# Optimization experiments

Measured on AMD Instinct MI355X. Metric: run time of the kernel, lower is better.

Reference implementation:

```python
import jax, jax.numpy as jnp
import numpy as np

N_PRO, N_WAT, E = 60000, 40000, 1000000
N = N_PRO + N_WAT
IN_DIM, HID, HEADS = 21, 32, 4
EDGE_K, EDGE_DIM = 32, 32
RADIUS_MAX = 5.0
FF_HID, OUT_DIM = 128, 2
HC = HID * HEADS


def setup_inputs() -> dict:
    key = jax.random.key(0)
    ks = jax.random.split(key, 32)

    def glorot(k, shape):
        fan = shape[0] + shape[-1]
        return jax.random.normal(k, shape, jnp.float32) * jnp.sqrt(2.0 / fan)

    inp = {
        'protein_pos': jax.random.normal(ks[0], (N_PRO, 3), jnp.float32),
        'water_pos': jax.random.normal(ks[1], (N_WAT, 3), jnp.float32),
        'protein_features': jax.random.uniform(ks[2], (N_PRO, IN_DIM), jnp.float32),
        'edge_index': jax.random.randint(ks[3], (2, E), 0, N, jnp.int64),
        'gamma': jnp.array([10.0], jnp.float32),
        # feature_emb
        'Wf': glorot(ks[4], (IN_DIM, HID)), 'bf': jnp.zeros((HID,), jnp.float32),
        # edge_emb
        'We': glorot(ks[5], (EDGE_K, EDGE_DIM)), 'be': jnp.zeros((EDGE_DIM,), jnp.float32),
        # conv1 (in: HID)
        'W1': glorot(ks[6], (HID, HC)),
        'att_src1': glorot(ks[7], (HEADS, HID)), 'att_dst1': glorot(ks[8], (HEADS, HID)),
        'Wedge1': glorot(ks[9], (EDGE_DIM, HC)), 'att_edge1': glorot(ks[10], (HEADS, HID)),
        'b1': jnp.zeros((HC,), jnp.float32),
        # conv2 (in: HC)
        'W2': glorot(ks[11], (HC, HC)),
        'att_src2': glorot(ks[12], (HEADS, HID)), 'att_dst2': glorot(ks[13], (HEADS, HID)),
        'Wedge2': glorot(ks[14], (EDGE_DIM, HC)), 'att_edge2': glorot(ks[15], (HEADS, HID)),
        'b2': jnp.zeros((HC,), jnp.float32),
        # mlp
        'Wm1': glorot(ks[16], (HC, FF_HID)), 'bm1': jnp.zeros((FF_HID,), jnp.float32),
        'Wm2': glorot(ks[17], (FF_HID, OUT_DIM)), 'bm2': jnp.zeros((OUT_DIM,), jnp.float32),
    }
    return inp


def gat_conv(h, edge_attr, src, dst, W, att_s, att_d, Wedge, att_e, b):
    # h: [N, Din] -> x: [N, H, C]; edge features only modulate attention logits.
    x = (h @ W).reshape(N, HEADS, HID)
    e = (edge_attr @ Wedge).reshape(-1, HEADS, HID)
    a_s = jnp.einsum('nhc,hc->nh', x, att_s)   # [N,H]
    a_d = jnp.einsum('nhc,hc->nh', x, att_d)   # [N,H]
    a_e = jnp.einsum('ehc,hc->eh', e, att_e)   # [E,H]
    alpha = jax.nn.leaky_relu(a_s[src] + a_d[dst] + a_e, 0.2)  # [E,H]
    # segment softmax over incoming edges of each dst node
    m = jax.ops.segment_max(alpha, dst, num_segments=N)
    m = jnp.where(jnp.isfinite(m), m, 0.0)
    ex = jnp.exp(alpha - m[dst])
    den = jax.ops.segment_sum(ex, dst, num_segments=N)
    coef = ex / (den[dst] + 1e-16)             # [E,H]
    msg = x[src] * coef[:, :, None]            # [E,H,C]
    out = jax.ops.segment_sum(msg, dst, num_segments=N)  # [N,H,C]
    return out.reshape(N, HC) + b


def reference(protein_pos, water_pos, protein_features, edge_index, gamma,
              Wf, bf, We, be,
              W1, att_src1, att_dst1, Wedge1, att_edge1, b1,
              W2, att_src2, att_dst2, Wedge2, att_edge2, b2,
              Wm1, bm1, Wm2, bm2):
    pos = jnp.concatenate([protein_pos, water_pos], axis=0)  # [N,3]
    src, dst = edge_index[0], edge_index[1]
    edge_vec = pos[dst] - pos[src]
    edge_dis = jnp.linalg.norm(edge_vec, axis=-1)            # [E]
    # RBF expansion of distances
    centers = jnp.linspace(0.0, RADIUS_MAX, EDGE_K)
    edge_h = jnp.exp(-gamma[0] * (edge_dis[:, None] - centers[None, :]) ** 2)  # [E,K]
    edge_attr = edge_h @ We + be                             # [E,EDGE_DIM]

    # water nodes get one-hot 'water' feature in last slot
    water_feat = jnp.zeros((N_WAT, IN_DIM), protein_features.dtype).at[:, -1].set(1.0)
    feats = jnp.concatenate([protein_features, water_feat], axis=0)
    h = feats @ Wf + bf                                      # [N,HID]

    h = jax.nn.elu(gat_conv(h, edge_attr, src, dst, W1, att_src1, att_dst1, Wedge1, att_edge1, b1))
    h = jax.nn.elu(gat_conv(h, edge_attr, src, dst, W2, att_src2, att_dst2, Wedge2, att_edge2, b2))

    h = jax.nn.relu(h @ Wm1 + bm1) @ Wm2 + bm2               # [N,OUT_DIM]
    return h[N_PRO:]                                         # water nodes only
```

## Files before the change

kernel.cpp:

```cpp
#include <hip/hip_runtime.h>
#include <hip/hip_fp16.h>
#include <stdint.h>

#define N_PRO 60000
#define N_WAT 40000
#define NN    100000
#define NNP   100032
#define NE    1000000
#define IN_DIM 21
#define HID    32
#define HEADS  4
#define HC     128
#define EDGE_K 32
#define LUTN   2048
#define NH0B  ((NNP * 32) / 256)
#define NBUCK 196
#define EPT   4
#define SCATB ((NE / EPT + 255) / 256)
#define FCAP  6144
#define SLOTS (NBUCK * FCAP)
#define GSTRIDE 16

typedef _Float16 half8 __attribute__((ext_vector_type(8)));
typedef float    f32x4 __attribute__((ext_vector_type(4)));

__global__ __launch_bounds__(256) void k_pre(
    const float* We, const float* be,
    const float* Wedge1, const float* atte1,
    const float* Wedge2, const float* atte2,
    const float* Wf, const float* bfv,
    const float* W1, const float* atts1, const float* attd1,
    const float* gamma,
    float* smallw, float* lut, __half* w1h, int* gcur)
{
    __shared__ float V[2][128];
    __shared__ float aebs[4];
    int t = threadIdx.x;
    if (blockIdx.x == 16) {
        {
            int l = t >> 7, dh = t & 127, d = dh >> 2, h = dh & 3;
            const float* Wg = l ? Wedge2 : Wedge1;
            const float* ae = l ? atte2 : atte1;
            float s = 0.f;
            for (int c = 0; c < HID; c++)
                s += Wg[d * HC + h * HID + c] * ae[h * HID + c];
            V[l][dh] = s;
        }
        __syncthreads();
        {
            int l = t >> 7, kh = t & 127, k = kh >> 2, h = kh & 3;
            float s = 0.f;
            for (int d = 0; d < 32; d++)
                s += We[k * 32 + d] * V[l][d * 4 + h];
            smallw[(l ? 132 : 0) + kh] = s;
        }
        if (t < 8) {
            int l = t >> 2, h = t & 3;
            float s = 0.f;
            for (int d = 0; d < 32; d++)
                s += be[d] * V[l][d * 4 + h];
            smallw[(l ? 260 : 128) + h] = s;
        }
        if (t >= 32 && t < 64) {
            int c = t - 32;
            smallw[264 + c] = Wf[20 * 32 + c] + bfv[c];
        }
        {
            int side = t >> 7;
            int h = (t >> 5) & 3, c = t & 31;
            const float* av = side ? attd1 : atts1;
            float s = 0.f;
            for (int j = 0; j < 32; j++)
                s += W1[c * 128 + h * 32 + j] * av[h * 32 + j];
            smallw[(side ? 424 : 296) + (t & 127)] = s;
        }
        for (int i = t; i < 128 * 8; i += 256) {
            int c = i & 127, k4 = (i >> 7) * 4;
            float w0 = W1[(k4 + 0) * 128 + c];
            float w1v = W1[(k4 + 1) * 128 + c];
            float w2 = W1[(k4 + 2) * 128 + c];
            float w3 = W1[(k4 + 3) * 128 + c];
            __half2 p0 = __floats2half2_rn(w0, w1v);
            __half2 p1 = __floats2half2_rn(w2, w3);
            uint2 pk;
            pk.x = *(unsigned*)&p0;
            pk.y = *(unsigned*)&p1;
            *(uint2*)&w1h[c * 40 + k4] = pk;
        }
        for (int i = t; i < NBUCK * GSTRIDE; i += 256) gcur[i] = 0;
        return;
    }
    int e = blockIdx.x * 256 + t;
    int layer = e >> 11, bin = e & (LUTN - 1);
    const float* Wg = layer ? Wedge2 : Wedge1;
    const float* ae = layer ? atte2 : atte1;
    if (t < 128) {
        int d = t >> 2, h = t & 3;
        float s = 0.f;
        for (int c = 0; c < 32; c++)
            s += Wg[d * HC + h * HID + c] * ae[h * HID + c];
        V[0][t] = s;
    }
    __syncthreads();
    if (t < 128) {
        int k = t >> 2, h = t & 3;
        float s = 0.f;
        for (int d = 0; d < 32; d++)
            s += We[k * 32 + d] * V[0][d * 4 + h];
        V[1][t] = s;
    }
    if (t >= 128 && t < 132) {
        int h = t - 128;
        float s = 0.f;
        for (int d = 0; d < 32; d++)
            s += be[d] * V[0][d * 4 + h];
        aebs[h] = s;
    }
    __syncthreads();
    const float* U = V[1];
    float dd = bin * (1.0f / 256.0f);
    float g = gamma[0];
    float a0 = aebs[0], a1 = aebs[1], a2 = aebs[2], a3 = aebs[3];
    const float step = 5.0f / 31.0f;
    #pragma unroll
    for (int k = 0; k < EDGE_K; k++) {
        float tt = dd - (float)k * step;
        float r = __expf(-g * tt * tt);
        a0 += r * U[k * 4 + 0];
        a1 += r * U[k * 4 + 1];
        a2 += r * U[k * 4 + 2];
        a3 += r * U[k * 4 + 3];
    }
    *(float4*)&lut[(size_t)e * 4] = make_float4(a0, a1, a2, a3);
}

__global__ __launch_bounds__(256) void k_hs(
    const float* __restrict__ pf, const float* __restrict__ Wf,
    const float* __restrict__ bfv, const float* __restrict__ smallw,
    const int* __restrict__ ei, const float* __restrict__ ppos,
    const float* __restrict__ wpos, int* __restrict__ gcur,
    uint2* __restrict__ ebuf2,
    __half* __restrict__ h0, float* __restrict__ asd)
{
    int t = threadIdx.x;
    if (blockIdx.x < SCATB) {
        __shared__ int lh[256];
        __shared__ int lbase[256];
        lh[t] = 0;
        __syncthreads();
        int e0 = (blockIdx.x * 256 + t) * EPT;
        int bkt[EPT], rnk[EPT];
        unsigned rec0[EPT], rec1[EPT];
        #pragma unroll
        for (int j = 0; j < EPT; j++) bkt[j] = -1;
        if (e0 < NE) {
            int4 sa = *(const int4*)&ei[e0];
            int4 da = *(const int4*)&ei[NE + e0];
            int ss[4] = {sa.x, sa.y, sa.z, sa.w};
            int ds[4] = {da.x, da.y, da.z, da.w};
            #pragma unroll
            for (int j = 0; j < EPT; j++) {
                int s = ss[j], d = ds[j];
                if ((unsigned)d < (unsigned)NN) {
                    const float* ps = (s < N_PRO) ? &ppos[s * 3] : &wpos[(s - N_PRO) * 3];
                    const float* pd = (d < N_PRO) ? &ppos[d * 3] : &wpos[(d - N_PRO) * 3];
                    float dx = pd[0] - ps[0];
                    float dy = pd[1] - ps[1];
                    float dz = pd[2] - ps[2];
                    float dist = sqrtf(dx * dx + dy * dy + dz * dz);
                    unsigned code = (unsigned)fminf(dist * 4096.0f, 32767.0f);
                    bkt[j] = d >> 9;
                    rec0[j] = ((unsigned)d << 15) | code;
                    rec1[j] = (unsigned)s;
                    rnk[j] = atomicAdd(&lh[bkt[j]], 1);
                }
            }
        }
        __syncthreads();
        if (t < NBUCK)
            lbase[t] = lh[t] ? atomicAdd(&gcur[t * GSTRIDE], lh[t]) : 0;
        __syncthreads();
        #pragma unroll
        for (int j = 0; j < EPT; j++)
            if (bkt[j] >= 0) {
                int p = lbase[bkt[j]] + rnk[j];
                if (p < FCAP)
                    ebuf2[(size_t)bkt[j] * FCAP + p] = make_uint2(rec0[j], rec1[j]);
            }
        return;
    }
    __shared__ float Wfs[IN_DIM * 32];
    __shared__ float bfs[32];
    __shared__ float h0w[32];
    __shared__ float vas[128], vad[128];
    for (int i = t; i < IN_DIM * 32; i += 256) Wfs[i] = Wf[i];
    if (t < 32) { bfs[t] = bfv[t]; h0w[t] = smallw[264 + t]; }
    if (t < 128) vas[t] = smallw[296 + t];
    else         vad[t - 128] = smallw[424 + (t - 128)];
    __syncthreads();
    int id = (blockIdx.x - SCATB) * 256 + t;
    int n = id >> 5, c = id & 31;
    if (n >= NNP) return;
    float v;
    if (n < N_PRO) {
        float s = bfs[c];
        for (int k = 0; k < IN_DIM; k++)
            s += pf[n * IN_DIM + k] * Wfs[k * 32 + c];
        v = s;
    } else {
        v = h0w[c];
    }
    h0[(size_t)n * 32 + c] = __float2half(v);
    float ps[4], pd[4];
    #pragma unroll
    for (int h = 0; h < 4; h++) {
        ps[h] = v * vas[h * 32 + c];
        pd[h] = v * vad[h * 32 + c];
    }
    #pragma unroll
    for (int m = 1; m < 32; m <<= 1) {
        #pragma unroll
        for (int h = 0; h < 4; h++) {
            ps[h] += __shfl_xor(ps[h], m, 64);
            pd[h] += __shfl_xor(pd[h], m, 64);
        }
    }
    if ((t & 31) == 0) {
        *(float4*)&asd[(size_t)n * 8]     = make_float4(ps[0], ps[1], ps[2], ps[3]);
        *(float4*)&asd[(size_t)n * 8 + 4] = make_float4(pd[0], pd[1], pd[2], pd[3]);
    }
}

__global__ __launch_bounds__(1024) void k_fine(
    const int* __restrict__ gcur, const uint2* __restrict__ ebuf2,
    const float* __restrict__ lutg, const float* __restrict__ asd,
    int* __restrict__ offA, int* __restrict__ offE,
    unsigned* __restrict__ e4, float* __restrict__ wb)
{
    __shared__ uint2 eL[FCAP];
    __shared__ int lcnt[512], lexc[512];
    __shared__ int wsum[8];
    int b = blockIdx.x, t = threadIdx.x;
    int beg = b * FCAP;
    int nb = gcur[b * GSTRIDE];
    if (nb > FCAP) nb = FCAP;
    for (int i = t; i < nb; i += 1024) eL[i] = ebuf2[beg + i];
    if (t < 512) lcnt[t] = 0;
    __syncthreads();
    for (int i = t; i < nb; i += 1024)
        atomicAdd(&lcnt[(eL[i].x >> 15) & 511], 1);
    __syncthreads();
    int c = 0;
    if (t < 512) {
        c = lcnt[t];
        int lane = t & 63;
        int v = c;
        #pragma unroll
        for (int d = 1; d < 64; d <<= 1) {
            int x = __shfl_up(v, d, 64);
            if (lane >= d) v += x;
        }
        if (lane == 63) wsum[t >> 6] = v;
        lexc[t] = v - c;
    }
    __syncthreads();
    if (t < 8) {
        int orig = wsum[t];
        int v = orig;
        #pragma unroll
        for (int d = 1; d < 8; d <<= 1) {
            int x = __shfl_up(v, d, 64);
            if (t >= d) v += x;
        }
        wsum[t] = v - orig;
    }
    __syncthreads();
    if (t < 512) {
        lexc[t] += wsum[t >> 6];
        int node = b * 512 + t;
        if (node < NN) {
            offA[node] = beg + lexc[t];
            offE[node] = beg + lexc[t] + c;
        }
        lcnt[t] = 0;
    }
    __syncthreads();
    for (int i = t; i < nb; i += 1024) {
        uint2 u = eL[i];
        int ln = (int)((u.x >> 15) & 511u);
        int r = atomicAdd(&lcnt[ln], 1);
        int p = beg + lexc[ln] + r;
        unsigned code = u.x & 32767u;
        unsigned s = u.y;
        e4[p] = (s << 15) | code;
        int n = (b << 9) + ln;
        float f = fminf((float)code * 0.0625f, (float)(LUTN - 2));
        int i0 = (int)f;
        float fr = f - (float)i0;
        float4 A = *(const float4*)&lutg[(size_t)i0 * 4];
        float4 B = *(const float4*)&lutg[(size_t)(i0 + 1) * 4];
        float4 as4 = *(const float4*)&asd[(size_t)s * 8];
        float4 ad4 = *(const float4*)&asd[(size_t)n * 8 + 4];
        float v0 = as4.x + ad4.x + A.x + (B.x - A.x) * fr;
        float v1 = as4.y + ad4.y + A.y + (B.y - A.y) * fr;
        float v2 = as4.z + ad4.z + A.z + (B.z - A.z) * fr;
        float v3 = as4.w + ad4.w + A.w + (B.w - A.w) * fr;
        v0 = fmaxf(v0, 0.2f * v0);
        v1 = fmaxf(v1, 0.2f * v1);
        v2 = fmaxf(v2, 0.2f * v2);
        v3 = fmaxf(v3, 0.2f * v3);
        *(float4*)&wb[(size_t)p * 4] = make_float4(
            __expf(v0), __expf(v1), __expf(v2), __expf(v3));
    }
}

__global__ __launch_bounds__(256) void k_xm(
    const __half* __restrict__ h, const float* __restrict__ Wg,
    const float* __restrict__ atts, const float* __restrict__ attd,
    __half* __restrict__ x16, float* __restrict__ asd)
{
    __shared__ __half Wt[128 * 136];
    __shared__ float attS[128], attD[128];
    int t = threadIdx.x;
    for (int i = t; i < 128 * 32; i += 256) {
        int c = i & 127, d = (i >> 7) * 4;
        float w0 = Wg[(d + 0) * 128 + c];
        float w1 = Wg[(d + 1) * 128 + c];
        float w2 = Wg[(d + 2) * 128 + c];
        float w3 = Wg[(d + 3) * 128 + c];
        __half2 p0 = __floats2half2_rn(w0, w1);
        __half2 p1 = __floats2half2_rn(w2, w3);
        uint2 pk;
        pk.x = *(unsigned*)&p0;
        pk.y = *(unsigned*)&p1;
        *(uint2*)&Wt[c * 136 + d] = pk;
    }
    if (t < 128) { attS[t] = atts[t]; attD[t] = attd[t]; }
    __syncthreads();
    int wv = t >> 6, lane = t & 63;
    int m16 = lane & 15, quad = lane >> 4;
    int n0 = blockIdx.x * 64 + wv * 16;
    f32x4 acc[8];
    #pragma unroll
    for (int ct = 0; ct < 8; ct++) acc[ct] = (f32x4){0.f, 0.f, 0.f, 0.f};
    #pragma unroll
    for (int ks = 0; ks < 4; ks++) {
        int d0 = ks * 32 + quad * 8;
        half8 bf = *(const half8*)&h[(size_t)(n0 + m16) * 128 + d0];
        #pragma unroll
        for (int ct = 0; ct < 8; ct++) {
            half8 af = *(const half8*)&Wt[(ct * 16 + m16) * 136 + d0];
            acc[ct] = __builtin_amdgcn_mfma_f32_16x16x32_f16(af, bf, acc[ct], 0, 0, 0);
        }
    }
    __half* xrow = &x16[(size_t)(n0 + m16) * 128 + quad * 4];
    float ps[4] = {0.f, 0.f, 0.f, 0.f}, pd[4] = {0.f, 0.f, 0.f, 0.f};
    #pragma unroll
    for (int ct = 0; ct < 8; ct++) {
        f32x4 a = acc[ct];
        __half2 h0p = __floats2half2_rn(a[0], a[1]);
        __half2 h1p = __floats2half2_rn(a[2], a[3]);
        uint2 pk;
        pk.x = *(unsigned*)&h0p;
        pk.y = *(unsigned*)&h1p;
        *(uint2*)&xrow[ct * 16] = pk;
        int cb = ct * 16 + quad * 4;
        int hh = ct >> 1;
        ps[hh] += a[0] * attS[cb] + a[1] * attS[cb + 1]
                + a[2] * attS[cb + 2] + a[3] * attS[cb + 3];
        pd[hh] += a[0] * attD[cb] + a[1] * attD[cb + 1]
                + a[2] * attD[cb + 2] + a[3] * attD[cb + 3];
    }
    #pragma unroll
    for (int hh = 0; hh < 4; hh++) {
        ps[hh] += __shfl_xor(ps[hh], 16, 64);
        ps[hh] += __shfl_xor(ps[hh], 32, 64);
        pd[hh] += __shfl_xor(pd[hh], 16, 64);
        pd[hh] += __shfl_xor(pd[hh], 32, 64);
    }
    if (lane < 16) {
        int n = n0 + m16;
        *(float4*)&asd[(size_t)n * 8]     = make_float4(ps[0], ps[1], ps[2], ps[3]);
        *(float4*)&asd[(size_t)n * 8 + 4] = make_float4(pd[0], pd[1], pd[2], pd[3]);
    }
}

__global__ __launch_bounds__(256) void k_aggz(
    const int* __restrict__ offA, const int* __restrict__ offE,
    const unsigned* __restrict__ e4, const float* __restrict__ wb,
    const __half* __restrict__ h016, const __half* __restrict__ w1h,
    const float* __restrict__ b1, __half* __restrict__ hbuf)
{
    __shared__ __half Wt[128 * 40];
    __shared__ __half zs[16][136];
    int t = threadIdx.x;
    {
        uint4* dst = (uint4*)Wt;
        const uint4* src = (const uint4*)w1h;
        for (int i = t; i < 640; i += 256) dst[i] = src[i];
    }
    int wv = t >> 6, lane = t & 63;
    int g = lane >> 4, q = lane & 15;
    int n = blockIdx.x * 16 + wv * 4 + g;
    int beg = offA[n], end = offE[n];
    const __half2* x2 = (const __half2*)h016;
    float a0x = 0.f, a0y = 0.f, a1x = 0.f, a1y = 0.f;
    float a2x = 0.f, a2y = 0.f, a3x = 0.f, a3y = 0.f;
    float l0 = 0.f, l1 = 0.f, l2 = 0.f, l3 = 0.f;
    int i = beg;
    for (; i + 3 < end; i += 4) {
        unsigned u0 = e4[i],     u1 = e4[i + 1];
        unsigned u2 = e4[i + 2], u3 = e4[i + 3];
        float4 w0 = *(const float4*)&wb[(size_t)i * 4];
        float4 w1 = *(const float4*)&wb[(size_t)(i + 1) * 4];
        float4 w2 = *(const float4*)&wb[(size_t)(i + 2) * 4];
        float4 w3 = *(const float4*)&wb[(size_t)(i + 3) * 4];
        float2 x0 = __half22float2(x2[(u0 >> 15) * 16u + q]);
        float2 x1 = __half22float2(x2[(u1 >> 15) * 16u + q]);
        float2 x2v = __half22float2(x2[(u2 >> 15) * 16u + q]);
        float2 x3 = __half22float2(x2[(u3 >> 15) * 16u + q]);
        a0x += w0.x * x0.x + w1.x * x1.x + w2.x * x2v.x + w3.x * x3.x;
        a0y += w0.x * x0.y + w1.x * x1.y + w2.x * x2v.y + w3.x * x3.y;
        a1x += w0.y * x0.x + w1.y * x1.x + w2.y * x2v.x + w3.y * x3.x;
        a1y += w0.y * x0.y + w1.y * x1.y + w2.y * x2v.y + w3.y * x3.y;
        a2x += w0.z * x0.x + w1.z * x1.x + w2.z * x2v.x + w3.z * x3.x;
        a2y += w0.z * x0.y + w1.z * x1.y + w2.z * x2v.y + w3.z * x3.y;
        a3x += w0.w * x0.x + w1.w * x1.x + w2.w * x2v.x + w3.w * x3.x;
        a3y += w0.w * x0.y + w1.w * x1.y + w2.w * x2v.y + w3.w * x3.y;
        l0 += (w0.x + w1.x) + (w2.x + w3.x);
        l1 += (w0.y + w1.y) + (w2.y + w3.y);
        l2 += (w0.z + w1.z) + (w2.z + w3.z);
        l3 += (w0.w + w1.w) + (w2.w + w3.w);
    }
    for (; i < end; i++) {
        unsigned u0 = e4[i];
        float4 w0 = *(const float4*)&wb[(size_t)i * 4];
        float2 x0 = __half22float2(x2[(u0 >> 15) * 16u + q]);
        a0x += w0.x * x0.x;  a0y += w0.x * x0.y;
        a1x += w0.y * x0.x;  a1y += w0.y * x0.y;
        a2x += w0.z * x0.x;  a2y += w0.z * x0.y;
        a3x += w0.w * x0.x;  a3y += w0.w * x0.y;
        l0 += w0.x; l1 += w0.y; l2 += w0.z; l3 += w0.w;
    }
    float i0v = 1.0f / (l0 + 1e-16f);
    float i1v = 1.0f / (l1 + 1e-16f);
    float i2v = 1.0f / (l2 + 1e-16f);
    float i3v = 1.0f / (l3 + 1e-16f);
    int nl = wv * 4 + g;
    *(__half2*)&zs[nl][     q * 2] = __floats2half2_rn(a0x * i0v, a0y * i0v);
    *(__half2*)&zs[nl][32 + q * 2] = __floats2half2_rn(a1x * i1v, a1y * i1v);
    *(__half2*)&zs[nl][64 + q * 2] = __floats2half2_rn(a2x * i2v, a2y * i2v);
    *(__half2*)&zs[nl][96 + q * 2] = __floats2half2_rn(a3x * i3v, a3y * i3v);
    __syncthreads();
    int m16 = lane & 15, quad = lane >> 4;
    half8 bf = *(const half8*)&zs[m16][wv * 32 + quad * 8];
    __half* orow = &hbuf[(size_t)(blockIdx.x * 16 + m16) * 128 + quad * 4];
    #pragma unroll
    for (int c2 = 0; c2 < 2; c2++) {
        int ct = wv * 2 + c2;
        half8 af = *(const half8*)&Wt[(ct * 16 + m16) * 40 + quad * 8];
        f32x4 acc = __builtin_amdgcn_mfma_f32_16x16x32_f16(
            af, bf, (f32x4){0.f, 0.f, 0.f, 0.f}, 0, 0, 0);
        int cb = ct * 16 + quad * 4;
        float4 bb = *(const float4*)&b1[cb];
        float r0 = acc[0] + bb.x;
        float r1 = acc[1] + bb.y;
        float r2 = acc[2] + bb.z;
        float r3 = acc[3] + bb.w;
        r0 = r0 > 0.f ? r0 : __expf(r0) - 1.0f;
        r1 = r1 > 0.f ? r1 : __expf(r1) - 1.0f;
        r2 = r2 > 0.f ? r2 : __expf(r2) - 1.0f;
        r3 = r3 > 0.f ? r3 : __expf(r3) - 1.0f;
        __half2 ha = __floats2half2_rn(r0, r1);
        __half2 hb = __floats2half2_rn(r2, r3);
        uint2 pk;
        pk.x = *(unsigned*)&ha;
        pk.y = *(unsigned*)&hb;
        *(uint2*)&orow[ct * 16] = pk;
    }
}

__global__ __launch_bounds__(256) void k_agg2(
    const int* __restrict__ offA, const int* __restrict__ offE,
    const unsigned* __restrict__ e4,
    const float* __restrict__ lutg, const float* __restrict__ asd,
    const __half* __restrict__ x16, const float* __restrict__ bias,
    __half* __restrict__ hout)
{
    int t = threadIdx.x;
    int wv = t >> 6, lane = t & 63;
    int g = lane >> 5, q = lane & 31;
    int n = N_PRO + blockIdx.x * 8 + wv * 2 + g;
    int h = q >> 3;
    int beg = offA[n], end = offE[n];
    float adh = asd[(size_t)n * 8 + 4 + h];
    float ax = 0.f, ay = 0.f, az = 0.f, aw = 0.f, ls = 0.f;
    int i = beg;
    for (; i + 3 < end; i += 4) {
        unsigned uu[4];
        float ww[4];
        float2 rr[4];
        #pragma unroll
        for (int j = 0; j < 4; j++) uu[j] = e4[i + j];
        #pragma unroll
        for (int j = 0; j < 4; j++) {
            unsigned s = uu[j] >> 15;
            float f = fminf((float)(uu[j] & 32767u) * 0.0625f, (float)(LUTN - 2));
            int i0 = (int)f;
            float fr = f - (float)i0;
            float A = lutg[i0 * 4 + h], B = lutg[(i0 + 1) * 4 + h];
            float as0 = asd[(size_t)s * 8 + h];
            rr[j] = *(const float2*)&x16[(size_t)s * 128 + q * 4];
            float v = as0 + adh + A + (B - A) * fr;
            v = fmaxf(v, 0.2f * v);
            ww[j] = __expf(v);
        }
        #pragma unroll
        for (int j = 0; j < 4; j++) {
            float2 fa = __half22float2(*(__half2*)&rr[j].x);
            float2 fb = __half22float2(*(__half2*)&rr[j].y);
            ax += ww[j] * fa.x;
            ay += ww[j] * fa.y;
            az += ww[j] * fb.x;
            aw += ww[j] * fb.y;
            ls += ww[j];
        }
    }
    for (; i < end; i++) {
        unsigned u0 = e4[i];
        unsigned s0 = u0 >> 15;
        float f0 = fminf((float)(u0 & 32767u) * 0.0625f, (float)(LUTN - 2));
        int i00 = (int)f0;
        float fr0 = f0 - (float)i00;
        float A0 = lutg[i00 * 4 + h], B0 = lutg[(i00 + 1) * 4 + h];
        float as0 = asd[(size_t)s0 * 8 + h];
        float2 r0 = *(const float2*)&x16[(size_t)s0 * 128 + q * 4];
        float v0 = as0 + adh + A0 + (B0 - A0) * fr0;
        v0 = fmaxf(v0, 0.2f * v0);
        float w0 = __expf(v0);
        float2 f00 = __half22float2(*(__half2*)&r0.x);
        float2 f01 = __half22float2(*(__half2*)&r0.y);
        ax += w0 * f00.x; ay += w0 * f00.y;
        az += w0 * f01.x; aw += w0 * f01.y;
        ls += w0;
    }
    float inv = 1.0f / (ls + 1e-16f);
    float4 bb = *(const float4*)&bias[q * 4];
    float o0 = ax * inv + bb.x;
    float o1 = ay * inv + bb.y;
    float o2 = az * inv + bb.z;
    float o3 = aw * inv + bb.w;
    o0 = o0 > 0.f ? o0 : __expf(o0) - 1.0f;
    o1 = o1 > 0.f ? o1 : __expf(o1) - 1.0f;
    o2 = o2 > 0.f ? o2 : __expf(o2) - 1.0f;
    o3 = o3 > 0.f ? o3 : __expf(o3) - 1.0f;
    __half2 ha = __floats2half2_rn(o0, o1);
    __half2 hb = __floats2half2_rn(o2, o3);
    uint2 pk;
    pk.x = *(unsigned*)&ha;
    pk.y = *(unsigned*)&hb;
    *(uint2*)&hout[(size_t)n * 128 + q * 4] = pk;
}

__global__ __launch_bounds__(256) void k_mlp(
    const __half* __restrict__ hh, const float* __restrict__ Wm1,
    const float* __restrict__ bm1, const float* __restrict__ Wm2,
    const float* __restrict__ bm2, float* __restrict__ out)
{
    __shared__ __half Wt[128 * 136];
    __shared__ float b1s[128];
    __shared__ float w2s[256];
    int t = threadIdx.x;
    for (int i = t; i < 128 * 32; i += 256) {
        int c = i & 127, d = (i >> 7) * 4;
        float w0 = Wm1[(d + 0) * 128 + c];
        float w1 = Wm1[(d + 1) * 128 + c];
        float w2 = Wm1[(d + 2) * 128 + c];
        float w3 = Wm1[(d + 3) * 128 + c];
        __half2 p0 = __floats2half2_rn(w0, w1);
        __half2 p1 = __floats2half2_rn(w2, w3);
        uint2 pk;
        pk.x = *(unsigned*)&p0;
        pk.y = *(unsigned*)&p1;
        *(uint2*)&Wt[c * 136 + d] = pk;
    }
    if (t < 128) b1s[t] = bm1[t];
    w2s[t] = Wm2[t];
    __syncthreads();
    int wv = t >> 6, lane = t & 63;
    int m16 = lane & 15, quad = lane >> 4;
    int n0 = blockIdx.x * 64 + wv * 16;
    f32x4 acc[8];
    #pragma unroll
    for (int ct = 0; ct < 8; ct++) acc[ct] = (f32x4){0.f, 0.f, 0.f, 0.f};
    #pragma unroll
    for (int ks = 0; ks < 4; ks++) {
        int d0 = ks * 32 + quad * 8;
        half8 bf = *(const half8*)&hh[(size_t)(N_PRO + n0 + m16) * 128 + d0];
        #pragma unroll
        for (int ct = 0; ct < 8; ct++) {
            half8 af = *(const half8*)&Wt[(ct * 16 + m16) * 136 + d0];
            acc[ct] = __builtin_amdgcn_mfma_f32_16x16x32_f16(af, bf, acc[ct], 0, 0, 0);
        }
    }
    float p0 = 0.f, p1 = 0.f;
    #pragma unroll
    for (int ct = 0; ct < 8; ct++) {
        int cb = ct * 16 + quad * 4;
        float4 bb = *(const float4*)&b1s[cb];
        float r0 = fmaxf(acc[ct][0] + bb.x, 0.f);
        float r1 = fmaxf(acc[ct][1] + bb.y, 0.f);
        float r2 = fmaxf(acc[ct][2] + bb.z, 0.f);
        float r3 = fmaxf(acc[ct][3] + bb.w, 0.f);
        p0 += r0 * w2s[(cb + 0) * 2] + r1 * w2s[(cb + 1) * 2]
            + r2 * w2s[(cb + 2) * 2] + r3 * w2s[(cb + 3) * 2];
        p1 += r0 * w2s[(cb + 0) * 2 + 1] + r1 * w2s[(cb + 1) * 2 + 1]
            + r2 * w2s[(cb + 2) * 2 + 1] + r3 * w2s[(cb + 3) * 2 + 1];
    }
    p0 += __shfl_xor(p0, 16, 64);
    p0 += __shfl_xor(p0, 32, 64);
    p1 += __shfl_xor(p1, 16, 64);
    p1 += __shfl_xor(p1, 32, 64);
    if (lane < 16) {
        int wn = n0 + m16;
        *(float2*)&out[(size_t)wn * 2] = make_float2(p0 + bm2[0], p1 + bm2[1]);
    }
}

extern "C" void kernel_launch(void* const* d_in, const int* in_sizes, int n_in,
                              void* d_out, int out_size, void* d_ws, size_t ws_size,
                              hipStream_t stream)
{
    const float* ppos   = (const float*)d_in[0];
    const float* wpos   = (const float*)d_in[1];
    const float* pfeat  = (const float*)d_in[2];
    const int*   ei     = (const int*)d_in[3];
    const float* gamma  = (const float*)d_in[4];
    const float* Wf     = (const float*)d_in[5];
    const float* bfv    = (const float*)d_in[6];
    const float* We     = (const float*)d_in[7];
    const float* be     = (const float*)d_in[8];
    const float* W1     = (const float*)d_in[9];
    const float* atts1  = (const float*)d_in[10];
    const float* attd1  = (const float*)d_in[11];
    const float* Wedge1 = (const float*)d_in[12];
    const float* atte1  = (const float*)d_in[13];
    const float* b1     = (const float*)d_in[14];
    const float* W2     = (const float*)d_in[15];
    const float* atts2  = (const float*)d_in[16];
    const float* attd2  = (const float*)d_in[17];
    const float* Wedge2 = (const float*)d_in[18];
    const float* atte2  = (const float*)d_in[19];
    const float* b2     = (const float*)d_in[20];
    const float* Wm1    = (const float*)d_in[21];
    const float* bm1    = (const float*)d_in[22];
    const float* Wm2    = (const float*)d_in[23];
    const float* bm2    = (const float*)d_in[24];
    float* out = (float*)d_out;

    char* ws = (char*)d_ws;
    size_t o = 0;
    auto alloc = [&](size_t bytes) -> char* {
        char* p = ws + o;
        o += (bytes + 255) & ~(size_t)255;
        return p;
    };
    __half*   h0      = (__half*)alloc((size_t)NNP * 32 * 2);
    __half*   x16     = (__half*)alloc((size_t)NNP * 128 * 2);
    __half*   hbuf    = (__half*)alloc((size_t)NNP * 128 * 2);
    float*    asd     = (float*)alloc((size_t)NNP * 8 * 4);
    float*    wb      = (float*)alloc((size_t)SLOTS * 4 * 4);
    int*      offA    = (int*)alloc((size_t)NN * 4);
    int*      offE    = (int*)alloc((size_t)NN * 4);
    unsigned* e4      = (unsigned*)alloc((size_t)SLOTS * 4);
    int*      gcur    = (int*)alloc((size_t)NBUCK * GSTRIDE * 4);
    float*    smallw  = (float*)alloc(4096);
    float*    lutbuf  = (float*)alloc((size_t)2 * LUTN * 4 * 4);
    __half*   w1h     = (__half*)alloc((size_t)128 * 40 * 2);
    uint2*    ebuf2   = (uint2*)hbuf;

    k_pre<<<17, 256, 0, stream>>>(We, be, Wedge1, atte1, Wedge2, atte2, Wf, bfv,
                                  W1, atts1, attd1, gamma,
                                  smallw, lutbuf, w1h, gcur);
    k_hs<<<NH0B + SCATB, 256, 0, stream>>>(pfeat, Wf, bfv, smallw, ei, ppos, wpos,
                                           gcur, ebuf2, h0, asd);
    k_fine<<<NBUCK, 1024, 0, stream>>>(gcur, ebuf2, lutbuf, asd, offA, offE, e4, wb);
    k_aggz<<<NN / 16, 256, 0, stream>>>(offA, offE, e4, wb, h0, w1h, b1, hbuf);
    k_xm<<<NNP / 64, 256, 0, stream>>>(hbuf, W2, atts2, attd2, x16, asd);
    k_agg2<<<N_WAT / 8, 256, 0, stream>>>(offA, offE, e4,
                                          lutbuf + (size_t)LUTN * 4, asd, x16, b2, hbuf);
    k_mlp<<<N_WAT / 64, 256, 0, stream>>>(hbuf, Wm1, bm1, Wm2, bm2, out);
}
```

Measured before the change: 286.8 us.

## Stage bucketed edge records in shared memory for coalesced scatter writes

The edge bucketing pass now handles eight edges per thread instead of four. Each block computes an exclusive prefix sum over its per-bucket counts and sorts its records into shared memory by bucket. It then writes them out so that consecutive threads store to consecutive slots within each bucket, replacing the per-edge random global stores. This adds a block scan, extra shared memory and barriers, and halves the number of scatter blocks, in return for more coalesced writes to the bucket buffer.

```diff
diff --git a/kernel.cpp b/kernel.cpp
--- a/kernel.cpp
+++ b/kernel.cpp
@@ -15,8 +15,9 @@
 #define LUTN   2048
 #define NH0B  ((NNP * 32) / 256)
 #define NBUCK 196
-#define EPT   4
+#define EPT   8
 #define SCATB ((NE / EPT + 255) / 256)
+#define BEDGE (256 * EPT)
 #define FCAP  6144
 #define SLOTS (NBUCK * FCAP)
 #define GSTRIDE 16
@@ -145,7 +146,12 @@
     int t = threadIdx.x;
     if (blockIdx.x < SCATB) {
         __shared__ int lh[256];
+        __shared__ int lpre[256];
         __shared__ int lbase[256];
+        __shared__ int wsum4[4];
+        __shared__ int sTot;
+        __shared__ uint2 eS[BEDGE];
+        __shared__ short bS[BEDGE];
         lh[t] = 0;
         __syncthreads();
         int e0 = (blockIdx.x * 256 + t) * EPT;
@@ -155,9 +161,11 @@
         for (int j = 0; j < EPT; j++) bkt[j] = -1;
         if (e0 < NE) {
             int4 sa = *(const int4*)&ei[e0];
+            int4 sb = *(const int4*)&ei[e0 + 4];
             int4 da = *(const int4*)&ei[NE + e0];
-            int ss[4] = {sa.x, sa.y, sa.z, sa.w};
-            int ds[4] = {da.x, da.y, da.z, da.w};
+            int4 db = *(const int4*)&ei[NE + e0 + 4];
+            int ss[8] = {sa.x, sa.y, sa.z, sa.w, sb.x, sb.y, sb.z, sb.w};
+            int ds[8] = {da.x, da.y, da.z, da.w, db.x, db.y, db.z, db.w};
             #pragma unroll
             for (int j = 0; j < EPT; j++) {
                 int s = ss[j], d = ds[j];
@@ -177,16 +185,44 @@
             }
         }
         __syncthreads();
+        {
+            int c = lh[t];
+            int lane = t & 63, wv = t >> 6;
+            int v = c;
+            #pragma unroll
+            for (int d = 1; d < 64; d <<= 1) {
+                int x = __shfl_up(v, d, 64);
+                if (lane >= d) v += x;
+            }
+            if (lane == 63) wsum4[wv] = v;
+            lpre[t] = v - c;
+            __syncthreads();
+            if (t == 0) {
+                int s = 0;
+                #pragma unroll
+                for (int k = 0; k < 4; k++) { int x = wsum4[k]; wsum4[k] = s; s += x; }
+                sTot = s;
+            }
+            __syncthreads();
+            lpre[t] += wsum4[wv];
+        }
         if (t < NBUCK)
             lbase[t] = lh[t] ? atomicAdd(&gcur[t * GSTRIDE], lh[t]) : 0;
-        __syncthreads();
         #pragma unroll
         for (int j = 0; j < EPT; j++)
             if (bkt[j] >= 0) {
-                int p = lbase[bkt[j]] + rnk[j];
-                if (p < FCAP)
-                    ebuf2[(size_t)bkt[j] * FCAP + p] = make_uint2(rec0[j], rec1[j]);
+                int idx = lpre[bkt[j]] + rnk[j];
+                eS[idx] = make_uint2(rec0[j], rec1[j]);
+                bS[idx] = (short)bkt[j];
             }
+        __syncthreads();
+        int tot = sTot;
+        for (int i = t; i < tot; i += 256) {
+            int b = bS[i];
+            int p = lbase[b] + (i - lpre[b]);
+            if (p < FCAP)
+                ebuf2[(size_t)b * FCAP + p] = eS[i];
+        }
         return;
     }
     __shared__ float Wfs[IN_DIM * 32];
```

Result: faster. 280.9 us (-2.1%).
